# Optimization experiments

Hardware: AMD Instinct MI355X
Metric: run time of the kernel (lower is better)

Reference implementation:

```python
import jax, jax.numpy as jnp
import numpy as np

B, TV, TE = 128, 32, 64
VOCAB, EMB, H, REPR, NET, MAXLEN = 1024, 256, 512, 128, 8, 32


def setup_inputs() -> dict:
    key = jax.random.key(0)
    ks = jax.random.split(key, 26)
    g = lambda i, shape: jax.random.normal(ks[i], shape, dtype=jnp.float32) * 0.05
    return dict(
        input_vertex=jax.random.randint(ks[0], (B, TV), 0, VOCAB),
        input_edge=jax.random.randint(ks[1], (B, TE, 3), 0, NET),
        vertex_emb=g(2, (VOCAB, EMB)),
        v_Wi=g(3, (3 * H, EMB)), v_Wh=g(4, (3 * H, H)), v_bi=g(5, (3 * H,)), v_bh=g(6, (3 * H,)),
        vout_W=g(7, (VOCAB, H)), vout_b=g(8, (VOCAB,)),
        vrep_W=g(9, (REPR, H)), vrep_b=g(10, (REPR,)),
        edge_emb=g(11, (MAXLEN, EMB)),
        e_Wi=g(12, (3 * H, 2 * EMB)), e_Wh=g(13, (3 * H, H)), e_bi=g(14, (3 * H,)), e_bh=g(15, (3 * H,)),
        erep_W=g(16, (REPR, H)), erep_b=g(17, (REPR,)),
        etype_W=g(18, (NET, REPR)), etype_b=g(19, (NET,)),
        src_w=g(20, (REPR,)), src_b=g(21, ()),
        dst_w=g(22, (REPR,)), dst_b=g(23, ()),
    )


def _gru_scan(X, Wi, Wh, bi, bh):
    # X: [T, B, D] -> hidden states [T, B, H]; torch GRUCell gate order r,z,n
    gi = jnp.einsum('tbd,gd->tbg', X, Wi) + bi  # precompute input projections
    h0 = jnp.zeros((X.shape[1], Wh.shape[1]), X.dtype)

    def step(h, gi_t):
        gh = h @ Wh.T + bh
        ir, iz, inn = jnp.split(gi_t, 3, axis=-1)
        hr, hz, hn = jnp.split(gh, 3, axis=-1)
        r = jax.nn.sigmoid(ir + hr)
        z = jax.nn.sigmoid(iz + hz)
        n = jnp.tanh(inn + r * hn)
        h_new = (1.0 - z) * n + z * h
        return h_new, h_new

    _, hs = jax.lax.scan(step, h0, gi)
    return hs


def reference(input_vertex, input_edge, vertex_emb, v_Wi, v_Wh, v_bi, v_bh,
              vout_W, vout_b, vrep_W, vrep_b, edge_emb, e_Wi, e_Wh, e_bi, e_bh,
              erep_W, erep_b, etype_W, etype_b, src_w, src_b, dst_w, dst_b):
    # ---- vertex RNN ----
    Ve = vertex_emb[input_vertex].transpose(1, 0, 2)          # [Tv, B, emb]
    hv = _gru_scan(Ve, v_Wi, v_Wh, v_bi, v_bh)                # [Tv, B, H]
    O_vertex = jnp.einsum('tbh,vh->bvt', hv, vout_W) + vout_b[None, :, None]  # [B, vocab, Tv]
    vrep = jnp.einsum('tbh,rh->tbr', hv, vrep_W) + vrep_b     # [Tv, B, repr]

    # ---- edge RNN ----
    E = jnp.concatenate([edge_emb[input_edge[:, :, 0]],
                         edge_emb[input_edge[:, :, 1]]], axis=2)  # [B, Te, 2*emb]
    he = _gru_scan(E.transpose(1, 0, 2), e_Wi, e_Wh, e_bi, e_bh)  # [Te, B, H]
    e = jnp.einsum('tbh,rh->tbr', he, erep_W) + erep_b            # [Te, B, repr]
    O_edge_type = jnp.einsum('ebr,kr->bke', e, etype_W) + etype_b[None, :, None]  # [B, n_et, Te]

    # ---- edge-vertex additive attention: tanh(e + v) ----
    u = jnp.tanh(e[:, None] + vrep[None])                     # [Te, Tv, B, repr]
    osrc = jnp.einsum('evbr,r->bve', u, src_w) + src_b        # [B, Tv, Te]
    odst = jnp.einsum('evbr,r->bve', u, dst_w) + dst_b        # [B, Tv, Te]
    O_edge = jnp.stack([osrc, odst], axis=2)                  # [B, Tv, 2, Te]

    return O_vertex, O_edge, O_edge_type
```

## Files before the change

### kernel.cpp

```cpp
#include <hip/hip_runtime.h>
#include <hip/hip_bf16.h>


typedef __bf16 bf16_t;
typedef bf16_t bf16x8 __attribute__((ext_vector_type(8)));
typedef bf16_t bf16x4 __attribute__((ext_vector_type(4)));
typedef float  f32x4  __attribute__((ext_vector_type(4)));

#define OFF_GIV  0ull
#define OFF_GIE  6291456ull
#define OFF_HV   18874368ull
#define OFF_HE   20971520ull
#define OFF_VREP 25165824ull
#define OFF_EREP 25690112ull
#define OFF_HBUF 26738688ull
#define FLAG_BYTE_OFF 54001664ull
#define GICNT_BYTE_OFF 54001920ull
#define OFF_CVT  27002880ull
#define CVT_VEMB  0ull
#define CVT_EEMB  262144ull
#define CVT_VWI   270336ull
#define CVT_EWI   663552ull
#define CVT_VWH   1449984ull
#define CVT_EWH   2236416ull
#define CVT_VOUT  3022848ull
#define CVT_VREPW 3547136ull
#define CVT_EREPW 3612672ull

#define OUT_OV 0ull
#define OUT_OE 4194304ull
#define OUT_OT 4718592ull

__device__ __forceinline__ float fsigmoid(float x) {
    float e = __builtin_amdgcn_exp2f(-x * 1.4426950408889634f);
    return __builtin_amdgcn_rcpf(1.0f + e);
}
__device__ __forceinline__ float ftanh(float x) {
    x = fminf(x, 15.0f);
    float e = __builtin_amdgcn_exp2f(x * 2.8853900817779268f);
    return (e - 1.0f) * __builtin_amdgcn_rcpf(e + 1.0f);
}

__global__ __launch_bounds__(256) void prep_kernel(
    const float* __restrict__ vemb, const float* __restrict__ eemb,
    const float* __restrict__ vwi,  const float* __restrict__ ewi,
    const float* __restrict__ vwh,  const float* __restrict__ ewh,
    const float* __restrict__ voutw, const float* __restrict__ vrepw,
    const float* __restrict__ erepw, bf16_t* __restrict__ cvt,
    int* __restrict__ gicnt)
{
    int blk = blockIdx.x;
    if (blk >= 3592) {
        if (threadIdx.x < 96) gicnt[threadIdx.x] = 0;
        return;
    }
    const float* src; bf16_t* dst; int lb;
    if (blk < 256)       { src = vemb;  dst = cvt + CVT_VEMB;  lb = blk; }
    else if (blk < 264)  { src = eemb;  dst = cvt + CVT_EEMB;  lb = blk - 256; }
    else if (blk < 648)  { src = vwi;   dst = cvt + CVT_VWI;   lb = blk - 264; }
    else if (blk < 1416) { src = ewi;   dst = cvt + CVT_EWI;   lb = blk - 648; }
    else if (blk < 2184) { src = vwh;   dst = cvt + CVT_VWH;   lb = blk - 1416; }
    else if (blk < 2952) { src = ewh;   dst = cvt + CVT_EWH;   lb = blk - 2184; }
    else if (blk < 3464) { src = voutw; dst = cvt + CVT_VOUT;  lb = blk - 2952; }
    else if (blk < 3528) { src = vrepw; dst = cvt + CVT_VREPW; lb = blk - 3464; }
    else                 { src = erepw; dst = cvt + CVT_EREPW; lb = blk - 3528; }
    int idx = lb * 1024 + threadIdx.x * 4;
    float4 v = *(const float4*)(src + idx);
    bf16x4 o;
    o[0] = (bf16_t)v.x; o[1] = (bf16_t)v.y; o[2] = (bf16_t)v.z; o[3] = (bf16_t)v.w;
    *(bf16x4*)(dst + idx) = o;
}

template<int GATHER, int K>
__device__ __forceinline__ void produce_gi(
    const bf16_t* __restrict__ W, const float* __restrict__ bias,
    bf16_t* __restrict__ C, const int* __restrict__ gidx,
    const bf16_t* __restrict__ emb, int* __restrict__ cnt, int bx, int nbase)
{
    constexpr int K32 = K / 32;
    const int tid = threadIdx.x, lane = tid & 63, wv = tid >> 6;
    const int r16 = lane & 15, quad = lane >> 4, koff = quad * 8;
    const int mbase = bx * 512 + wv * 64;

    const bf16_t* ap0[4];
    const bf16_t* ap1[4];
#pragma unroll
    for (int i = 0; i < 4; ++i) {
        int row = mbase + i * 16 + r16;
        int b = row & 127, t = row >> 7;
        if (GATHER == 1) {
            ap0[i] = emb + (size_t)gidx[b * 32 + t] * 256 + koff;
            ap1[i] = ap0[i];
        } else {
            int c = (b * 64 + t) * 3;
            ap0[i] = emb + (size_t)gidx[c] * 256 + koff;
            ap1[i] = emb + (size_t)gidx[c + 1] * 256 + koff;
        }
    }
    const bf16_t* bp[4];
#pragma unroll
    for (int j = 0; j < 4; ++j)
        bp[j] = W + (size_t)(nbase + j * 16 + r16) * K + koff;

    f32x4 acc[4][4];
#pragma unroll
    for (int i = 0; i < 4; ++i)
#pragma unroll
        for (int j = 0; j < 4; ++j) acc[i][j] = (f32x4){0.f, 0.f, 0.f, 0.f};

    for (int kc = 0; kc < K32; ++kc) {
        bf16x8 a[4], b[4];
#pragma unroll
        for (int i = 0; i < 4; ++i) {
            const bf16_t* p;
            if (GATHER == 2) p = (kc < 8) ? (ap0[i] + kc * 32) : (ap1[i] + (kc - 8) * 32);
            else             p = ap0[i] + kc * 32;
            a[i] = *(const bf16x8*)p;
        }
#pragma unroll
        for (int j = 0; j < 4; ++j) b[j] = *(const bf16x8*)(bp[j] + kc * 32);
#pragma unroll
        for (int i = 0; i < 4; ++i)
#pragma unroll
            for (int j = 0; j < 4; ++j)
                acc[i][j] = __builtin_amdgcn_mfma_f32_16x16x32_bf16(a[i], b[j], acc[i][j], 0, 0, 0);
    }

#pragma unroll
    for (int j = 0; j < 4; ++j) {
        int col = nbase + j * 16 + r16;
        float bf = bias[col];
#pragma unroll
        for (int i = 0; i < 4; ++i) {
#pragma unroll
            for (int q = 0; q < 4; ++q) {
                int row = mbase + i * 16 + quad * 4 + q;
                bf16_t hb = (bf16_t)(acc[i][j][q] + bf);
                __hip_atomic_store((unsigned short*)(C + (size_t)row * 1536 + col),
                                   __builtin_bit_cast(unsigned short, hb),
                                   __ATOMIC_RELAXED, __HIP_MEMORY_SCOPE_AGENT);
            }
        }
    }
    __builtin_amdgcn_s_waitcnt(0);
    __syncthreads();
    if (tid < 4)
        __hip_atomic_fetch_add(&cnt[bx * 4 + tid], 1,
                               __ATOMIC_RELAXED, __HIP_MEMORY_SCOPE_AGENT);
}

__global__ __launch_bounds__(512) void fused_scan(
    bf16_t* __restrict__ giV, bf16_t* __restrict__ giE,
    const bf16_t* __restrict__ WhV, const bf16_t* __restrict__ WhE,
    const float* __restrict__ bhV, const float* __restrict__ bhE,
    bf16_t* __restrict__ hV, bf16_t* __restrict__ hE,
    bf16_t* __restrict__ hbuf, int* __restrict__ flags, int* __restrict__ gicnt,
    const int* __restrict__ ivtx, const int* __restrict__ iedg,
    const bf16_t* __restrict__ vemb, const bf16_t* __restrict__ eemb,
    const bf16_t* __restrict__ vwi, const bf16_t* __restrict__ ewi,
    const float* __restrict__ vbi, const float* __restrict__ ebi)
{
    __shared__ __align__(16) bf16_t hbf[2][16][520];
    const int bid = blockIdx.x;

    if (bid >= 64) {
        if (bid < 256) {
            int g2 = bid - 64;
            produce_gi<1, 256>(vwi, vbi, giV, ivtx, vemb, gicnt, g2 & 7, (g2 >> 3) * 64);
        } else {
            int g3 = bid - 256;
            produce_gi<2, 512>(ewi, ebi, giE, iedg, eemb, gicnt + 32, g3 & 15, (g3 >> 4) * 64);
        }
        return;
    }

    const int role = bid >> 5;
    const int lb   = bid & 31;
    const int g    = lb & 7;
    const int s    = lb >> 3;
    const bf16_t* gi = role ? giE : giV;
    const bf16_t* Wh = role ? WhE : WhV;
    const float*  bh = role ? bhE : bhV;
    bf16_t* hout = role ? hE : hV;
    const int T = role ? 64 : 32;
    const int slot = role * 8 + g;
    bf16_t* buf0 = hbuf + (size_t)slot * 2 * 8192;
    int* fl = flags + slot * 4;
    int* gc = role ? (gicnt + 32) : gicnt;
    const int bb = g * 16;

    const int tid = threadIdx.x, lane = tid & 63, wv = tid >> 6;
    const int r16 = lane & 15, quad = lane >> 4, koff = quad * 8;
    const int j = s * 128 + wv * 16 + r16;
    const int rs0 = (s + 1) & 3, rs1 = (s + 2) & 3, rs2 = (s + 3) & 3;

    bf16x8 wfrag[3][16];
#pragma unroll
    for (int gate = 0; gate < 3; ++gate) {
        const bf16_t* wrow = Wh + ((size_t)(gate * 512 + j)) * 512 + koff;
#pragma unroll
        for (int kc = 0; kc < 16; ++kc)
            wfrag[gate][kc] = *(const bf16x8*)(wrow + kc * 32);
    }
    const float bhr = bh[j], bhz = bh[512 + j], bhn = bh[1024 + j];
    float hq[4] = {0.f, 0.f, 0.f, 0.f};

    for (int i = tid; i < 16 * 512; i += 512)
        hbf[0][i >> 9][i & 511] = (bf16_t)0.f;

    const int arow = tid >> 5, au = tid & 31;

    for (int t = 0; t < T; ++t) {
        while (__hip_atomic_load(&gc[t], __ATOMIC_RELAXED,
                                 __HIP_MEMORY_SCOPE_AGENT) < 24) { }
        asm volatile("" ::: "memory");
        float gv[3][4];
#pragma unroll
        for (int gg = 0; gg < 3; ++gg)
#pragma unroll
            for (int q = 0; q < 4; ++q)
                gv[gg][q] = (float)gi[((size_t)(t * 128 + bb + quad * 4 + q)) * 1536
                                      + gg * 512 + j];

        if (t > 0) {
            while (!__all((int)(__hip_atomic_load(&fl[lane & 3], __ATOMIC_RELAXED,
                                                  __HIP_MEMORY_SCOPE_AGENT) >= t))) { }
            asm volatile("" ::: "memory");
            unsigned long long* src = (unsigned long long*)(buf0 + (size_t)(t & 1) * 8192);
            unsigned long long vv[3];
            vv[0] = __hip_atomic_load(src + arow * 128 + rs0 * 32 + au, __ATOMIC_RELAXED, __HIP_MEMORY_SCOPE_AGENT);
            vv[1] = __hip_atomic_load(src + arow * 128 + rs1 * 32 + au, __ATOMIC_RELAXED, __HIP_MEMORY_SCOPE_AGENT);
            vv[2] = __hip_atomic_load(src + arow * 128 + rs2 * 32 + au, __ATOMIC_RELAXED, __HIP_MEMORY_SCOPE_AGENT);
            *(unsigned long long*)&hbf[t & 1][arow][rs0 * 128 + au * 4] = vv[0];
            *(unsigned long long*)&hbf[t & 1][arow][rs1 * 128 + au * 4] = vv[1];
            *(unsigned long long*)&hbf[t & 1][arow][rs2 * 128 + au * 4] = vv[2];
        }
        __syncthreads();

        const bf16_t (*cur)[520] = hbf[t & 1];
        f32x4 ar = {0.f,0.f,0.f,0.f}, az = {0.f,0.f,0.f,0.f}, an = {0.f,0.f,0.f,0.f};
#pragma unroll
        for (int kc = 0; kc < 16; ++kc) {
            bf16x8 a = *(const bf16x8*)&cur[r16][kc * 32 + koff];
            ar = __builtin_amdgcn_mfma_f32_16x16x32_bf16(a, wfrag[0][kc], ar, 0, 0, 0);
            az = __builtin_amdgcn_mfma_f32_16x16x32_bf16(a, wfrag[1][kc], az, 0, 0, 0);
            an = __builtin_amdgcn_mfma_f32_16x16x32_bf16(a, wfrag[2][kc], an, 0, 0, 0);
        }

        bf16_t hb4[4];
#pragma unroll
        for (int q = 0; q < 4; ++q) {
            float r = fsigmoid(gv[0][q] + ar[q] + bhr);
            float z = fsigmoid(gv[1][q] + az[q] + bhz);
            float n = ftanh(gv[2][q] + r * (an[q] + bhn));
            float hnew = (1.0f - z) * n + z * hq[q];
            hq[q] = hnew;
            hb4[q] = (bf16_t)hnew;
        }

        bf16_t (*nxt)[520] = hbf[(t + 1) & 1];
#pragma unroll
        for (int q = 0; q < 4; ++q) nxt[quad * 4 + q][j] = hb4[q];

        if (t + 1 < T) {
            bf16_t* dstg = buf0 + (size_t)((t + 1) & 1) * 8192;
#pragma unroll
            for (int q = 0; q < 4; ++q)
                __hip_atomic_store((unsigned short*)(dstg + (quad * 4 + q) * 512 + j),
                                   __builtin_bit_cast(unsigned short, hb4[q]),
                                   __ATOMIC_RELAXED, __HIP_MEMORY_SCOPE_AGENT);
            __builtin_amdgcn_s_waitcnt(0);
            __syncthreads();
            if (tid == 0)
                __hip_atomic_store(&fl[s], t + 1,
                                   __ATOMIC_RELAXED, __HIP_MEMORY_SCOPE_AGENT);
        } else {
            __syncthreads();
        }
#pragma unroll
        for (int q = 0; q < 4; ++q)
            hout[((size_t)((bb + quad * 4 + q) * T + t)) * 512 + j] = hb4[q];
    }
}

template<int OUTMODE, int K, int TT, typename CT>
__global__ __launch_bounds__(256) void gemm_bt(
    const bf16_t* __restrict__ A, const bf16_t* __restrict__ W,
    const float* __restrict__ bias, CT* __restrict__ C, int N)
{
    constexpr int K32 = K / 32;
    const int tid = threadIdx.x, lane = tid & 63, wv = tid >> 6;
    const int r16 = lane & 15, quad = lane >> 4, koff = quad * 8;
    const int mbase = blockIdx.x * 256 + wv * 64;
    const int nbase = blockIdx.y * 64;

    const bf16_t* ap0[4];
#pragma unroll
    for (int i = 0; i < 4; ++i)
        ap0[i] = A + (size_t)(mbase + i * 16 + r16) * K + koff;
    const bf16_t* bp[4];
#pragma unroll
    for (int j = 0; j < 4; ++j)
        bp[j] = W + (size_t)(nbase + j * 16 + r16) * K + koff;

    f32x4 acc[4][4];
#pragma unroll
    for (int i = 0; i < 4; ++i)
#pragma unroll
        for (int j = 0; j < 4; ++j) acc[i][j] = (f32x4){0.f, 0.f, 0.f, 0.f};

    for (int kc = 0; kc < K32; ++kc) {
        bf16x8 a[4], b[4];
#pragma unroll
        for (int i = 0; i < 4; ++i) a[i] = *(const bf16x8*)(ap0[i] + kc * 32);
#pragma unroll
        for (int j = 0; j < 4; ++j) b[j] = *(const bf16x8*)(bp[j] + kc * 32);
#pragma unroll
        for (int i = 0; i < 4; ++i)
#pragma unroll
            for (int j = 0; j < 4; ++j)
                acc[i][j] = __builtin_amdgcn_mfma_f32_16x16x32_bf16(a[i], b[j], acc[i][j], 0, 0, 0);
    }

#pragma unroll
    for (int j = 0; j < 4; ++j) {
        int col = nbase + j * 16 + r16;
        float bf = bias[col];
#pragma unroll
        for (int i = 0; i < 4; ++i) {
            int rowq = mbase + i * 16 + quad * 4;
            if (OUTMODE == 1) {
                int b = rowq >> 5, t0 = rowq & 31;
                float4 v4;
                v4.x = acc[i][j][0] + bf; v4.y = acc[i][j][1] + bf;
                v4.z = acc[i][j][2] + bf; v4.w = acc[i][j][3] + bf;
                *(float4*)((float*)C + ((size_t)(b * 1024) + col) * 32 + t0) = v4;
            } else {
#pragma unroll
                for (int q = 0; q < 4; ++q)
                    C[(size_t)(rowq + q) * N + col] = (CT)(acc[i][j][q] + bf);
            }
        }
    }
}

__global__ __launch_bounds__(256) void etype_kernel(
    const bf16_t* __restrict__ erep, const float* __restrict__ W,
    const float* __restrict__ bias, float* __restrict__ out)
{
    int o = blockIdx.x * 256 + threadIdx.x;
    int te = o & 63, k = (o >> 6) & 7, b = o >> 9;
    float sacc = bias[k];
    const bf16_t* e = erep + ((size_t)(b * 64 + te)) * 128;
    const float* w = W + k * 128;
#pragma unroll 8
    for (int r = 0; r < 128; ++r) sacc += (float)e[r] * w[r];
    out[OUT_OT + o] = sacc;
}

__global__ __launch_bounds__(256) void attn_kernel(
    const bf16_t* __restrict__ erep, const bf16_t* __restrict__ vrep,
    const float* __restrict__ src_w, const float* __restrict__ src_b,
    const float* __restrict__ dst_w, const float* __restrict__ dst_b,
    float* __restrict__ out)
{
    int b = blockIdx.x >> 1, half = blockIdx.x & 1;
    __shared__ float es[32][129], vs[32][129], swf[128], dwf[128];
    int tid = threadIdx.x;
    for (int f = tid; f < 32 * 128; f += 256) {
        int i = f >> 7, r = f & 127;
        es[i][r] = (float)erep[((size_t)(b * 64 + half * 32 + i)) * 128 + r];
        vs[i][r] = (float)vrep[((size_t)(b * 32 + i)) * 128 + r];
    }
    if (tid < 128) { swf[tid] = src_w[tid]; dwf[tid] = dst_w[tid]; }
    __syncthreads();
    float sb = src_b[0], db = dst_b[0];
    for (int p = tid; p < 1024; p += 256) {
        int te = p & 31, tv = p >> 5;
        float sacc = 0.f, dacc = 0.f;
#pragma unroll 4
        for (int r = 0; r < 128; ++r) {
            float u = ftanh(es[te][r] + vs[tv][r]);
            sacc += u * swf[r];
            dacc += u * dwf[r];
        }
        int teg = half * 32 + te;
        size_t base = OUT_OE + ((size_t)(b * 32 + tv) * 2) * 64;
        out[base + teg]      = sacc + sb;
        out[base + 64 + teg] = dacc + db;
    }
}

extern "C" void kernel_launch(void* const* d_in, const int* in_sizes, int n_in,
                              void* d_out, int out_size, void* d_ws, size_t ws_size,
                              hipStream_t stream)
{
    const int*   input_vertex = (const int*)d_in[0];
    const int*   input_edge   = (const int*)d_in[1];
    const float* vertex_emb   = (const float*)d_in[2];
    const float* v_Wi  = (const float*)d_in[3];
    const float* v_Wh  = (const float*)d_in[4];
    const float* v_bi  = (const float*)d_in[5];
    const float* v_bh  = (const float*)d_in[6];
    const float* vout_W = (const float*)d_in[7];
    const float* vout_b = (const float*)d_in[8];
    const float* vrep_W = (const float*)d_in[9];
    const float* vrep_b = (const float*)d_in[10];
    const float* edge_emb = (const float*)d_in[11];
    const float* e_Wi  = (const float*)d_in[12];
    const float* e_Wh  = (const float*)d_in[13];
    const float* e_bi  = (const float*)d_in[14];
    const float* e_bh  = (const float*)d_in[15];
    const float* erep_W = (const float*)d_in[16];
    const float* erep_b = (const float*)d_in[17];
    const float* etype_W = (const float*)d_in[18];
    const float* etype_b = (const float*)d_in[19];
    const float* src_w = (const float*)d_in[20];
    const float* src_b = (const float*)d_in[21];
    const float* dst_w = (const float*)d_in[22];
    const float* dst_b = (const float*)d_in[23];

    bf16_t* ws   = (bf16_t*)d_ws;
    bf16_t* giV  = ws + OFF_GIV;
    bf16_t* giE  = ws + OFF_GIE;
    bf16_t* hV   = ws + OFF_HV;
    bf16_t* hE   = ws + OFF_HE;
    bf16_t* vrep = ws + OFF_VREP;
    bf16_t* erep = ws + OFF_EREP;
    bf16_t* hbuf = ws + OFF_HBUF;
    bf16_t* cvt  = ws + OFF_CVT;
    int*    flags = (int*)((char*)d_ws + FLAG_BYTE_OFF);
    int*    gicnt = (int*)((char*)d_ws + GICNT_BYTE_OFF);
    float*  out  = (float*)d_out;

    prep_kernel<<<3593, 256, 0, stream>>>(vertex_emb, edge_emb, v_Wi, e_Wi, v_Wh, e_Wh,
                                          vout_W, vrep_W, erep_W, cvt, gicnt);

    fused_scan<<<640, 512, 0, stream>>>(
        giV, giE, cvt + CVT_VWH, cvt + CVT_EWH, v_bh, e_bh, hV, hE,
        hbuf, flags, gicnt, input_vertex, input_edge,
        cvt + CVT_VEMB, cvt + CVT_EEMB, cvt + CVT_VWI, cvt + CVT_EWI,
        v_bi, e_bi);

    gemm_bt<1, 512, 32, float><<<dim3(16, 16), 256, 0, stream>>>(
        hV, cvt + CVT_VOUT, vout_b, out, 1024);
    gemm_bt<0, 512, 32, bf16_t><<<dim3(16, 2), 256, 0, stream>>>(
        hV, cvt + CVT_VREPW, vrep_b, vrep, 128);
    gemm_bt<0, 512, 64, bf16_t><<<dim3(32, 2), 256, 0, stream>>>(
        hE, cvt + CVT_EREPW, erep_b, erep, 128);

    etype_kernel<<<256, 256, 0, stream>>>(erep, etype_W, etype_b, out);
    attn_kernel<<<256, 256, 0, stream>>>(erep, vrep, src_w, src_b, dst_w, dst_b, out);
}
```

Before: 479.7 us.

## Fuse output GEMMs into scan kernel as flag-gated consumer blocks

```diff
diff --git a/kernel.cpp b/kernel.cpp
--- a/kernel.cpp
+++ b/kernel.cpp
@@ -51,7 +51,7 @@
 {
     int blk = blockIdx.x;
     if (blk >= 3592) {
-        if (threadIdx.x < 96) gicnt[threadIdx.x] = 0;
+        if (threadIdx.x < 128) gicnt[threadIdx.x] = 0;
         return;
     }
     const float* src; bf16_t* dst; int lb;
@@ -149,6 +149,68 @@
                                __ATOMIC_RELAXED, __HIP_MEMORY_SCOPE_AGENT);
 }
 
+template<int OUTMODE, int K>
+__device__ __forceinline__ void consume_gemm(
+    const bf16_t* __restrict__ A, const bf16_t* __restrict__ W,
+    const float* __restrict__ bias, void* __restrict__ Cv,
+    int N, int bx, int nbase)
+{
+    constexpr int K32 = K / 32;
+    const int tid = threadIdx.x, lane = tid & 63, wv = tid >> 6;
+    const int r16 = lane & 15, quad = lane >> 4, koff = quad * 8;
+    const int mbase = bx * 512 + wv * 64;
+
+    const bf16_t* ap[4];
+#pragma unroll
+    for (int i = 0; i < 4; ++i)
+        ap[i] = A + (size_t)(mbase + i * 16 + r16) * K + koff;
+    const bf16_t* bp[4];
+#pragma unroll
+    for (int j = 0; j < 4; ++j)
+        bp[j] = W + (size_t)(nbase + j * 16 + r16) * K + koff;
+
+    f32x4 acc[4][4];
+#pragma unroll
+    for (int i = 0; i < 4; ++i)
+#pragma unroll
+        for (int j = 0; j < 4; ++j) acc[i][j] = (f32x4){0.f, 0.f, 0.f, 0.f};
+
+    for (int kc = 0; kc < K32; ++kc) {
+        bf16x8 a[4], b[4];
+#pragma unroll
+        for (int i = 0; i < 4; ++i) a[i] = *(const bf16x8*)(ap[i] + kc * 32);
+#pragma unroll
+        for (int j = 0; j < 4; ++j) b[j] = *(const bf16x8*)(bp[j] + kc * 32);
+#pragma unroll
+        for (int i = 0; i < 4; ++i)
+#pragma unroll
+            for (int j = 0; j < 4; ++j)
+                acc[i][j] = __builtin_amdgcn_mfma_f32_16x16x32_bf16(a[i], b[j], acc[i][j], 0, 0, 0);
+    }
+
+#pragma unroll
+    for (int j = 0; j < 4; ++j) {
+        int col = nbase + j * 16 + r16;
+        float bf = bias[col];
+#pragma unroll
+        for (int i = 0; i < 4; ++i) {
+            int rowq = mbase + i * 16 + quad * 4;
+            if (OUTMODE == 1) {
+                int b = rowq >> 5, t0 = rowq & 31;
+                float4 v4;
+                v4.x = acc[i][j][0] + bf; v4.y = acc[i][j][1] + bf;
+                v4.z = acc[i][j][2] + bf; v4.w = acc[i][j][3] + bf;
+                *(float4*)((float*)Cv + ((size_t)(b * 1024) + col) * 32 + t0) = v4;
+            } else {
+                bf16_t* C = (bf16_t*)Cv;
+#pragma unroll
+                for (int q = 0; q < 4; ++q)
+                    C[(size_t)(rowq + q) * N + col] = (bf16_t)(acc[i][j][q] + bf);
+            }
+        }
+    }
+}
+
 __global__ __launch_bounds__(512) void fused_scan(
     bf16_t* __restrict__ giV, bf16_t* __restrict__ giE,
     const bf16_t* __restrict__ WhV, const bf16_t* __restrict__ WhE,
@@ -158,18 +220,44 @@
     const int* __restrict__ ivtx, const int* __restrict__ iedg,
     const bf16_t* __restrict__ vemb, const bf16_t* __restrict__ eemb,
     const bf16_t* __restrict__ vwi, const bf16_t* __restrict__ ewi,
-    const float* __restrict__ vbi, const float* __restrict__ ebi)
+    const float* __restrict__ vbi, const float* __restrict__ ebi,
+    const bf16_t* __restrict__ voutw, const float* __restrict__ voutb,
+    const bf16_t* __restrict__ vrepw, const float* __restrict__ vrepb,
+    const bf16_t* __restrict__ erepw, const float* __restrict__ erepb,
+    bf16_t* __restrict__ vrep, bf16_t* __restrict__ erep,
+    float* __restrict__ out)
 {
     __shared__ __align__(16) bf16_t hbf[2][16][520];
+    __shared__ char ldspad[31744];
     const int bid = blockIdx.x;
+    if ((int)gridDim.x < 0) ldspad[threadIdx.x] = 0;
 
     if (bid >= 64) {
         if (bid < 256) {
             int g2 = bid - 64;
             produce_gi<1, 256>(vwi, vbi, giV, ivtx, vemb, gicnt, g2 & 7, (g2 >> 3) * 64);
-        } else {
+        } else if (bid < 640) {
             int g3 = bid - 256;
             produce_gi<2, 512>(ewi, ebi, giE, iedg, eemb, gicnt + 32, g3 & 15, (g3 >> 4) * 64);
+        } else if (bid < 784) {
+            while (__hip_atomic_load(&gicnt[96], __ATOMIC_RELAXED,
+                                     __HIP_MEMORY_SCOPE_AGENT) < 32)
+                __builtin_amdgcn_s_sleep(8);
+            asm volatile("" ::: "memory");
+            if (bid < 768) {
+                int cb = bid - 640;
+                consume_gemm<1, 512>(hV, voutw, voutb, out, 1024, cb & 7, (cb >> 3) * 64);
+            } else {
+                int cb = bid - 768;
+                consume_gemm<0, 512>(hV, vrepw, vrepb, vrep, 128, cb & 7, (cb >> 3) * 64);
+            }
+        } else {
+            while (__hip_atomic_load(&gicnt[97], __ATOMIC_RELAXED,
+                                     __HIP_MEMORY_SCOPE_AGENT) < 32)
+                __builtin_amdgcn_s_sleep(8);
+            asm volatile("" ::: "memory");
+            int cb = bid - 784;
+            consume_gemm<0, 512>(hE, erepw, erepb, erep, 128, cb & 15, (cb >> 4) * 64);
         }
         return;
     }
@@ -187,6 +275,7 @@
     bf16_t* buf0 = hbuf + (size_t)slot * 2 * 8192;
     int* fl = flags + slot * 4;
     int* gc = role ? (gicnt + 32) : gicnt;
+    int* done = role ? &gicnt[97] : &gicnt[96];
     const int bb = g * 16;
 
     const int tid = threadIdx.x, lane = tid & 63, wv = tid >> 6;
@@ -279,69 +368,16 @@
         }
 #pragma unroll
         for (int q = 0; q < 4; ++q)
-            hout[((size_t)((bb + quad * 4 + q) * T + t)) * 512 + j] = hb4[q];
-    }
-}
-
-template<int OUTMODE, int K, int TT, typename CT>
-__global__ __launch_bounds__(256) void gemm_bt(
-    const bf16_t* __restrict__ A, const bf16_t* __restrict__ W,
-    const float* __restrict__ bias, CT* __restrict__ C, int N)
-{
-    constexpr int K32 = K / 32;
-    const int tid = threadIdx.x, lane = tid & 63, wv = tid >> 6;
-    const int r16 = lane & 15, quad = lane >> 4, koff = quad * 8;
-    const int mbase = blockIdx.x * 256 + wv * 64;
-    const int nbase = blockIdx.y * 64;
-
-    const bf16_t* ap0[4];
-#pragma unroll
-    for (int i = 0; i < 4; ++i)
-        ap0[i] = A + (size_t)(mbase + i * 16 + r16) * K + koff;
-    const bf16_t* bp[4];
-#pragma unroll
-    for (int j = 0; j < 4; ++j)
-        bp[j] = W + (size_t)(nbase + j * 16 + r16) * K + koff;
-
-    f32x4 acc[4][4];
-#pragma unroll
-    for (int i = 0; i < 4; ++i)
-#pragma unroll
-        for (int j = 0; j < 4; ++j) acc[i][j] = (f32x4){0.f, 0.f, 0.f, 0.f};
-
-    for (int kc = 0; kc < K32; ++kc) {
-        bf16x8 a[4], b[4];
-#pragma unroll
-        for (int i = 0; i < 4; ++i) a[i] = *(const bf16x8*)(ap0[i] + kc * 32);
-#pragma unroll
-        for (int j = 0; j < 4; ++j) b[j] = *(const bf16x8*)(bp[j] + kc * 32);
-#pragma unroll
-        for (int i = 0; i < 4; ++i)
-#pragma unroll
-            for (int j = 0; j < 4; ++j)
-                acc[i][j] = __builtin_amdgcn_mfma_f32_16x16x32_bf16(a[i], b[j], acc[i][j], 0, 0, 0);
-    }
-
-#pragma unroll
-    for (int j = 0; j < 4; ++j) {
-        int col = nbase + j * 16 + r16;
-        float bf = bias[col];
-#pragma unroll
-        for (int i = 0; i < 4; ++i) {
-            int rowq = mbase + i * 16 + quad * 4;
-            if (OUTMODE == 1) {
-                int b = rowq >> 5, t0 = rowq & 31;
-                float4 v4;
-                v4.x = acc[i][j][0] + bf; v4.y = acc[i][j][1] + bf;
-                v4.z = acc[i][j][2] + bf; v4.w = acc[i][j][3] + bf;
-                *(float4*)((float*)C + ((size_t)(b * 1024) + col) * 32 + t0) = v4;
-            } else {
-#pragma unroll
-                for (int q = 0; q < 4; ++q)
-                    C[(size_t)(rowq + q) * N + col] = (CT)(acc[i][j][q] + bf);
-            }
-        }
-    }
+            __hip_atomic_store(
+                (unsigned short*)(hout + ((size_t)((bb + quad * 4 + q) * T + t)) * 512 + j),
+                __builtin_bit_cast(unsigned short, hb4[q]),
+                __ATOMIC_RELAXED, __HIP_MEMORY_SCOPE_AGENT);
+    }
+
+    __builtin_amdgcn_s_waitcnt(0);
+    __syncthreads();
+    if (tid == 0)
+        __hip_atomic_fetch_add(done, 1, __ATOMIC_RELAXED, __HIP_MEMORY_SCOPE_AGENT);
 }
 
 __global__ __launch_bounds__(256) void etype_kernel(
@@ -436,18 +472,13 @@
     prep_kernel<<<3593, 256, 0, stream>>>(vertex_emb, edge_emb, v_Wi, e_Wi, v_Wh, e_Wh,
                                           vout_W, vrep_W, erep_W, cvt, gicnt);
 
-    fused_scan<<<640, 512, 0, stream>>>(
+    fused_scan<<<816, 512, 0, stream>>>(
         giV, giE, cvt + CVT_VWH, cvt + CVT_EWH, v_bh, e_bh, hV, hE,
         hbuf, flags, gicnt, input_vertex, input_edge,
         cvt + CVT_VEMB, cvt + CVT_EEMB, cvt + CVT_VWI, cvt + CVT_EWI,
-        v_bi, e_bi);
-
-    gemm_bt<1, 512, 32, float><<<dim3(16, 16), 256, 0, stream>>>(
-        hV, cvt + CVT_VOUT, vout_b, out, 1024);
-    gemm_bt<0, 512, 32, bf16_t><<<dim3(16, 2), 256, 0, stream>>>(
-        hV, cvt + CVT_VREPW, vrep_b, vrep, 128);
-    gemm_bt<0, 512, 64, bf16_t><<<dim3(32, 2), 256, 0, stream>>>(
-        hE, cvt + CVT_EREPW, erep_b, erep, 128);
+        v_bi, e_bi,
+        cvt + CVT_VOUT, vout_b, cvt + CVT_VREPW, vrep_b,
+        cvt + CVT_EREPW, erep_b, vrep, erep, out);
 
     etype_kernel<<<256, 256, 0, stream>>>(erep, etype_W, etype_b, out);
     attn_kernel<<<256, 256, 0, stream>>>(erep, vrep, src_w, src_b, dst_w, dst_b, out);
```

Result: faster. 456.0 us (-4.9%).
